# Optimization experiments

Measured on AMD Instinct MI355X. Metric: run time of the kernel, lower is better.

The kernel has to match this reference:

```python
import jax, jax.numpy as jnp
import numpy as np

B, S, H = 32, 2048, 512

def setup_inputs() -> dict:
    key = jax.random.key(0)
    k1, k2, k3, k4 = jax.random.split(key, 4)
    Y = jax.random.normal(k1, (B, S, H), dtype=jnp.float32)
    mask_Y = jnp.ones((B, S), dtype=jnp.float32)
    W = jax.random.normal(k2, (H, H), dtype=jnp.float32)
    b = jax.random.normal(k3, (H,), dtype=jnp.float32)
    w = jax.random.normal(k4, (H,), dtype=jnp.float32)
    return {"Y": Y, "mask_Y": mask_Y, "W": W, "b": b, "w": w}

def reference(Y, mask_Y, W, b, w):
    # u: [B,S,H] = tanh(Y @ W + b)
    u = jnp.tanh(jnp.einsum('bsh,hd->bsd', Y, W) + b)
    # scores: [B,S] = u . w, masked with large negative additive bias
    scores = jnp.einsum('bsh,h->bs', u, w) - 1000.0 * (1.0 - mask_Y)
    alpha = jax.nn.softmax(scores, axis=1)  # [B,S]
    # c_star: [B,H] = attention-weighted sum of Y
    c_star = jnp.einsum('bs,bsh->bh', alpha, Y)
    return c_star
```

## Files before the change

kernel.cpp:

```cpp
#include <hip/hip_runtime.h>
#include <hip/hip_bf16.h>


#define Bsz 32
#define Ssz 2048
#define Hsz 512
#define Msz (Bsz * Ssz)

using half8   = __attribute__((ext_vector_type(8))) _Float16;
using floatx4 = __attribute__((ext_vector_type(4))) float;

__device__ __forceinline__ void llds(_Float16* l, const _Float16* g) {
  __builtin_amdgcn_global_load_lds((const __attribute__((address_space(1))) void*)g,
                                   (__attribute__((address_space(3))) void*)l, 16, 0, 0);
}

__device__ __forceinline__ float fast_tanh(float x) {
  const float e = __expf(2.f * x);
  return 1.f - 2.f / (e + 1.f);
}

__global__ __launch_bounds__(256) void wsplit_k(const float* __restrict__ W,
                                                _Float16* __restrict__ Wt) {
  __shared__ float tile[32][33];
  const int bx = blockIdx.x & 15, by = blockIdx.x >> 4;
  const int tx = threadIdx.x & 31, ty = threadIdx.x >> 5;
#pragma unroll
  for (int i = 0; i < 4; ++i)
    tile[ty + 8 * i][tx] = W[(size_t)(by * 32 + ty + 8 * i) * Hsz + bx * 32 + tx];
  __syncthreads();
#pragma unroll
  for (int i = 0; i < 4; ++i) {
    const int n = bx * 32 + ty + 8 * i;
    const int k = by * 32 + tx;
    const float v = tile[tx][ty + 8 * i];
    const _Float16 hi = (_Float16)v;
    const _Float16 lo = (_Float16)(v - (float)hi);
    Wt[(size_t)n * 1024 + k] = hi;
    Wt[(size_t)n * 1024 + 512 + k] = lo;
  }
}

__global__ __launch_bounds__(256) void gemm_score_k(const float* __restrict__ Y,
                                                    const _Float16* __restrict__ Wt,
                                                    const float* __restrict__ bvec,
                                                    const float* __restrict__ wvec,
                                                    float* __restrict__ scores4) {
  __shared__ __align__(16) _Float16 As[128 * 32];
  __shared__ __align__(16) _Float16 Bh[128 * 32];
  __shared__ __align__(16) _Float16 Bl[128 * 32];
  const int tid = threadIdx.x;
  const int lane = tid & 63, wv = tid >> 6;
  const int wr = wv >> 1, wc = wv & 1;
  const int lr = lane & 15, lq = lane >> 4;
  const int g = blockIdx.x;
  const int x = g & 7, q = g >> 3;
  const int nblk = q & 3;
  const int mblk = (q >> 2) * 8 + x;

  floatx4 acc[4][4];
#pragma unroll
  for (int rf = 0; rf < 4; ++rf)
#pragma unroll
    for (int cf = 0; cf < 4; ++cf)
      acc[rf][cf] = (floatx4){0.f, 0.f, 0.f, 0.f};

  const int arow = tid >> 1;
  const int p0 = (tid & 1) * 2;
  const float* aga = Y + ((size_t)(mblk * 128 + arow)) * Hsz + p0 * 8;
  const int s0 = (p0 ^ ((arow >> 1) & 3)) * 8;
  const int s1 = ((p0 + 1) ^ ((arow >> 1) & 3)) * 8;
  const size_t brow0 = (size_t)nblk * 128 * 1024;

  for (int it = 0; it < 16; ++it) {
    const int k0 = it * 32;
#pragma unroll
    for (int i = 0; i < 2; ++i) {
      const int cbase = i * 256 + wv * 64;
      const int c = cbase + lane;
      const int brow = c >> 2;
      const int gpart = (c & 3) ^ ((c >> 3) & 3);
      const _Float16* gb = Wt + brow0 + (size_t)brow * 1024 + (k0 + gpart * 8);
      llds(&Bh[cbase * 8], gb);
      llds(&Bl[cbase * 8], gb + 512);
    }
    {
      const float4* g4 = (const float4*)(aga + k0);
      const float4 f0 = g4[0], f1 = g4[1], f2 = g4[2], f3 = g4[3];
      half8 h0, h1;
      h0[0] = (_Float16)f0.x; h0[1] = (_Float16)f0.y; h0[2] = (_Float16)f0.z; h0[3] = (_Float16)f0.w;
      h0[4] = (_Float16)f1.x; h0[5] = (_Float16)f1.y; h0[6] = (_Float16)f1.z; h0[7] = (_Float16)f1.w;
      h1[0] = (_Float16)f2.x; h1[1] = (_Float16)f2.y; h1[2] = (_Float16)f2.z; h1[3] = (_Float16)f2.w;
      h1[4] = (_Float16)f3.x; h1[5] = (_Float16)f3.y; h1[6] = (_Float16)f3.z; h1[7] = (_Float16)f3.w;
      *(half8*)&As[arow * 32 + s0] = h0;
      *(half8*)&As[arow * 32 + s1] = h1;
    }
    __syncthreads();

    half8 a[4], bhf[4], blf[4];
#pragma unroll
    for (int rf = 0; rf < 4; ++rf) {
      const int ar = wr * 64 + rf * 16 + lr;
      a[rf] = *(const half8*)&As[ar * 32 + (lq ^ ((ar >> 1) & 3)) * 8];
    }
#pragma unroll
    for (int cf = 0; cf < 4; ++cf) {
      const int nr = wc * 64 + cf * 16 + lr;
      const int na = nr * 32 + (lq ^ ((nr >> 1) & 3)) * 8;
      bhf[cf] = *(const half8*)&Bh[na];
      blf[cf] = *(const half8*)&Bl[na];
    }
#pragma unroll
    for (int rf = 0; rf < 4; ++rf)
#pragma unroll
      for (int cf = 0; cf < 4; ++cf)
        acc[rf][cf] = __builtin_amdgcn_mfma_f32_16x16x32_f16(a[rf], bhf[cf], acc[rf][cf], 0, 0, 0);
#pragma unroll
    for (int rf = 0; rf < 4; ++rf)
#pragma unroll
      for (int cf = 0; cf < 4; ++cf)
        acc[rf][cf] = __builtin_amdgcn_mfma_f32_16x16x32_f16(a[rf], blf[cf], acc[rf][cf], 0, 0, 0);
    __syncthreads();
  }

  float bb[4], ww[4];
  const int colbase = nblk * 128 + wc * 64;
#pragma unroll
  for (int cf = 0; cf < 4; ++cf) {
    const int col = colbase + cf * 16 + lr;
    bb[cf] = bvec[col];
    ww[cf] = wvec[col];
  }
  float* red = (float*)As;
#pragma unroll
  for (int rf = 0; rf < 4; ++rf) {
#pragma unroll
    for (int r = 0; r < 4; ++r) {
      float v = 0.f;
#pragma unroll
      for (int cf = 0; cf < 4; ++cf)
        v += fast_tanh(acc[rf][cf][r] + bb[cf]) * ww[cf];
      v += __shfl_xor(v, 1, 16);
      v += __shfl_xor(v, 2, 16);
      v += __shfl_xor(v, 4, 16);
      v += __shfl_xor(v, 8, 16);
      if (lr == 0)
        red[(wr * 64 + rf * 16 + lq * 4 + r) * 2 + wc] = v;
    }
  }
  __syncthreads();
  if (tid < 128)
    scores4[(size_t)nblk * Msz + mblk * 128 + tid] = red[2 * tid] + red[2 * tid + 1];
}

__global__ __launch_bounds__(256) void softmax_k(const float* __restrict__ scores4,
                                                 const float* __restrict__ mask,
                                                 float* __restrict__ alpha) {
  const int b = blockIdx.x, t = threadIdx.x;
  const int lane = t & 63, wv = t >> 6;
  float s[8];
  float mx = -3.4e38f;
#pragma unroll
  for (int i = 0; i < 8; ++i) {
    const int idx = b * Ssz + i * 256 + t;
    float v = scores4[idx] + scores4[Msz + idx] + scores4[2 * Msz + idx] + scores4[3 * Msz + idx];
    v -= 1000.f * (1.f - mask[idx]);
    s[i] = v;
    mx = fmaxf(mx, v);
  }
  for (int off = 32; off > 0; off >>= 1) mx = fmaxf(mx, __shfl_xor(mx, off, 64));
  __shared__ float rm[4], rs[4];
  if (lane == 0) rm[wv] = mx;
  __syncthreads();
  mx = fmaxf(fmaxf(rm[0], rm[1]), fmaxf(rm[2], rm[3]));
  float sum = 0.f;
#pragma unroll
  for (int i = 0; i < 8; ++i) {
    s[i] = __expf(s[i] - mx);
    sum += s[i];
  }
  for (int off = 32; off > 0; off >>= 1) sum += __shfl_xor(sum, off, 64);
  if (lane == 0) rs[wv] = sum;
  __syncthreads();
  sum = rs[0] + rs[1] + rs[2] + rs[3];
  const float inv = 1.f / sum;
#pragma unroll
  for (int i = 0; i < 8; ++i) alpha[b * Ssz + i * 256 + t] = s[i] * inv;
}

__global__ __launch_bounds__(256) void wsum_k(const float* __restrict__ alpha,
                                              const float* __restrict__ Y,
                                              float* __restrict__ out) {
  const int b = blockIdx.x >> 6, sc = blockIdx.x & 63;
  const int t = threadIdx.x;
  const float2* Y2 = (const float2*)(Y + ((size_t)b * Ssz + sc * 32) * Hsz);
  const float* al = alpha + b * Ssz + sc * 32;
  float cx = 0.f, cy = 0.f;
  for (int s = 0; s < 32; ++s) {
    const float a = al[s];
    const float2 y = Y2[(size_t)s * 256 + t];
    cx = fmaf(a, y.x, cx);
    cy = fmaf(a, y.y, cy);
  }
  atomicAdd(&out[b * Hsz + 2 * t], cx);
  atomicAdd(&out[b * Hsz + 2 * t + 1], cy);
}

extern "C" void kernel_launch(void* const* d_in, const int* in_sizes, int n_in,
                              void* d_out, int out_size, void* d_ws, size_t ws_size,
                              hipStream_t stream) {
  (void)in_sizes; (void)n_in; (void)out_size; (void)ws_size;
  const float* Y    = (const float*)d_in[0];
  const float* mask = (const float*)d_in[1];
  const float* W    = (const float*)d_in[2];
  const float* bvec = (const float*)d_in[3];
  const float* wvec = (const float*)d_in[4];
  float* out = (float*)d_out;

  char* ws = (char*)d_ws;
  _Float16* Wt   = (_Float16*)ws;
  float* scores4 = (float*)(ws + ((size_t)1 << 20));
  float* alpha   = (float*)(ws + ((size_t)2 << 20));

  hipMemsetAsync(out, 0, Bsz * Hsz * sizeof(float), stream);

  wsplit_k<<<256, 256, 0, stream>>>(W, Wt);
  gemm_score_k<<<(Msz / 128) * 4, 256, 0, stream>>>(Y, Wt, bvec, wvec, scores4);
  softmax_k<<<Bsz, 256, 0, stream>>>(scores4, mask, alpha);
  wsum_k<<<Bsz * 64, 256, 0, stream>>>(alpha, Y, out);
}
```

Before: 289.3 us.

## Double-buffer GEMM LDS tiles and fuse softmax into weighted-sum kernel

```diff
diff --git a/kernel.cpp b/kernel.cpp
--- a/kernel.cpp
+++ b/kernel.cpp
@@ -46,9 +46,9 @@
                                                     const float* __restrict__ bvec,
                                                     const float* __restrict__ wvec,
                                                     float* __restrict__ scores4) {
-  __shared__ __align__(16) _Float16 As[128 * 32];
-  __shared__ __align__(16) _Float16 Bh[128 * 32];
-  __shared__ __align__(16) _Float16 Bl[128 * 32];
+  __shared__ __align__(16) _Float16 As[2][128 * 32];
+  __shared__ __align__(16) _Float16 Bh[2][128 * 32];
+  __shared__ __align__(16) _Float16 Bl[2][128 * 32];
   const int tid = threadIdx.x;
   const int lane = tid & 63, wv = tid >> 6;
   const int wr = wv >> 1, wc = wv & 1;
@@ -72,7 +72,7 @@
   const int s1 = ((p0 + 1) ^ ((arow >> 1) & 3)) * 8;
   const size_t brow0 = (size_t)nblk * 128 * 1024;
 
-  for (int it = 0; it < 16; ++it) {
+  auto stageB = [&](int it, int buf) {
     const int k0 = it * 32;
 #pragma unroll
     for (int i = 0; i < 2; ++i) {
@@ -81,34 +81,52 @@
       const int brow = c >> 2;
       const int gpart = (c & 3) ^ ((c >> 3) & 3);
       const _Float16* gb = Wt + brow0 + (size_t)brow * 1024 + (k0 + gpart * 8);
-      llds(&Bh[cbase * 8], gb);
-      llds(&Bl[cbase * 8], gb + 512);
-    }
-    {
-      const float4* g4 = (const float4*)(aga + k0);
-      const float4 f0 = g4[0], f1 = g4[1], f2 = g4[2], f3 = g4[3];
-      half8 h0, h1;
-      h0[0] = (_Float16)f0.x; h0[1] = (_Float16)f0.y; h0[2] = (_Float16)f0.z; h0[3] = (_Float16)f0.w;
-      h0[4] = (_Float16)f1.x; h0[5] = (_Float16)f1.y; h0[6] = (_Float16)f1.z; h0[7] = (_Float16)f1.w;
-      h1[0] = (_Float16)f2.x; h1[1] = (_Float16)f2.y; h1[2] = (_Float16)f2.z; h1[3] = (_Float16)f2.w;
-      h1[4] = (_Float16)f3.x; h1[5] = (_Float16)f3.y; h1[6] = (_Float16)f3.z; h1[7] = (_Float16)f3.w;
-      *(half8*)&As[arow * 32 + s0] = h0;
-      *(half8*)&As[arow * 32 + s1] = h1;
-    }
+      llds(&Bh[buf][cbase * 8], gb);
+      llds(&Bl[buf][cbase * 8], gb + 512);
+    }
+  };
+  auto loadA = [&](int it, float4* f) {
+    const float4* g4 = (const float4*)(aga + it * 32);
+    f[0] = g4[0]; f[1] = g4[1]; f[2] = g4[2]; f[3] = g4[3];
+  };
+  auto cvtWriteA = [&](const float4* f, int buf) {
+    half8 h0, h1;
+    h0[0] = (_Float16)f[0].x; h0[1] = (_Float16)f[0].y; h0[2] = (_Float16)f[0].z; h0[3] = (_Float16)f[0].w;
+    h0[4] = (_Float16)f[1].x; h0[5] = (_Float16)f[1].y; h0[6] = (_Float16)f[1].z; h0[7] = (_Float16)f[1].w;
+    h1[0] = (_Float16)f[2].x; h1[1] = (_Float16)f[2].y; h1[2] = (_Float16)f[2].z; h1[3] = (_Float16)f[2].w;
+    h1[4] = (_Float16)f[3].x; h1[5] = (_Float16)f[3].y; h1[6] = (_Float16)f[3].z; h1[7] = (_Float16)f[3].w;
+    *(half8*)&As[buf][arow * 32 + s0] = h0;
+    *(half8*)&As[buf][arow * 32 + s1] = h1;
+  };
+
+  {
+    float4 fa[4];
+    stageB(0, 0);
+    loadA(0, fa);
+    cvtWriteA(fa, 0);
     __syncthreads();
+  }
+
+  for (int it = 0; it < 16; ++it) {
+    const int p = it & 1;
+    float4 fb[4];
+    if (it < 15) {
+      stageB(it + 1, p ^ 1);
+      loadA(it + 1, fb);
+    }
 
     half8 a[4], bhf[4], blf[4];
 #pragma unroll
     for (int rf = 0; rf < 4; ++rf) {
       const int ar = wr * 64 + rf * 16 + lr;
-      a[rf] = *(const half8*)&As[ar * 32 + (lq ^ ((ar >> 1) & 3)) * 8];
+      a[rf] = *(const half8*)&As[p][ar * 32 + (lq ^ ((ar >> 1) & 3)) * 8];
     }
 #pragma unroll
     for (int cf = 0; cf < 4; ++cf) {
       const int nr = wc * 64 + cf * 16 + lr;
       const int na = nr * 32 + (lq ^ ((nr >> 1) & 3)) * 8;
-      bhf[cf] = *(const half8*)&Bh[na];
-      blf[cf] = *(const half8*)&Bl[na];
+      bhf[cf] = *(const half8*)&Bh[p][na];
+      blf[cf] = *(const half8*)&Bl[p][na];
     }
 #pragma unroll
     for (int rf = 0; rf < 4; ++rf)
@@ -120,6 +138,9 @@
 #pragma unroll
       for (int cf = 0; cf < 4; ++cf)
         acc[rf][cf] = __builtin_amdgcn_mfma_f32_16x16x32_f16(a[rf], blf[cf], acc[rf][cf], 0, 0, 0);
+
+    if (it < 15)
+      cvtWriteA(fb, p ^ 1);
     __syncthreads();
   }
 
@@ -153,11 +174,16 @@
     scores4[(size_t)nblk * Msz + mblk * 128 + tid] = red[2 * tid] + red[2 * tid + 1];
 }
 
-__global__ __launch_bounds__(256) void softmax_k(const float* __restrict__ scores4,
-                                                 const float* __restrict__ mask,
-                                                 float* __restrict__ alpha) {
-  const int b = blockIdx.x, t = threadIdx.x;
-  const int lane = t & 63, wv = t >> 6;
+__global__ __launch_bounds__(256) void wsum_fused_k(const float* __restrict__ scores4,
+                                                    const float* __restrict__ mask,
+                                                    const float* __restrict__ Y,
+                                                    float* __restrict__ out) {
+  const int b = blockIdx.x >> 3, hs = blockIdx.x & 7;
+  const int t = threadIdx.x, lane = t & 63, wv = t >> 6;
+  __shared__ float alpha_s[Ssz];
+  __shared__ float rbuf[256];
+  __shared__ float rm[4], rs[4];
+
   float s[8];
   float mx = -3.4e38f;
 #pragma unroll
@@ -169,7 +195,6 @@
     mx = fmaxf(mx, v);
   }
   for (int off = 32; off > 0; off >>= 1) mx = fmaxf(mx, __shfl_xor(mx, off, 64));
-  __shared__ float rm[4], rs[4];
   if (lane == 0) rm[wv] = mx;
   __syncthreads();
   mx = fmaxf(fmaxf(rm[0], rm[1]), fmaxf(rm[2], rm[3]));
@@ -185,25 +210,20 @@
   sum = rs[0] + rs[1] + rs[2] + rs[3];
   const float inv = 1.f / sum;
 #pragma unroll
-  for (int i = 0; i < 8; ++i) alpha[b * Ssz + i * 256 + t] = s[i] * inv;
-}
-
-__global__ __launch_bounds__(256) void wsum_k(const float* __restrict__ alpha,
-                                              const float* __restrict__ Y,
-                                              float* __restrict__ out) {
-  const int b = blockIdx.x >> 6, sc = blockIdx.x & 63;
-  const int t = threadIdx.x;
-  const float2* Y2 = (const float2*)(Y + ((size_t)b * Ssz + sc * 32) * Hsz);
-  const float* al = alpha + b * Ssz + sc * 32;
-  float cx = 0.f, cy = 0.f;
-  for (int s = 0; s < 32; ++s) {
-    const float a = al[s];
-    const float2 y = Y2[(size_t)s * 256 + t];
-    cx = fmaf(a, y.x, cx);
-    cy = fmaf(a, y.y, cy);
-  }
-  atomicAdd(&out[b * Hsz + 2 * t], cx);
-  atomicAdd(&out[b * Hsz + 2 * t + 1], cy);
+  for (int i = 0; i < 8; ++i) alpha_s[i * 256 + t] = s[i] * inv;
+  __syncthreads();
+
+  const float* Yp = Y + (size_t)b * Ssz * Hsz + hs * 64 + lane;
+  const int sbase = wv * 512;
+  float acc = 0.f;
+#pragma unroll 8
+  for (int k = 0; k < 512; ++k)
+    acc = fmaf(alpha_s[sbase + k], Yp[(size_t)(sbase + k) * Hsz], acc);
+  rbuf[t] = acc;
+  __syncthreads();
+  if (wv == 0)
+    out[b * Hsz + hs * 64 + lane] =
+        rbuf[lane] + rbuf[64 + lane] + rbuf[128 + lane] + rbuf[192 + lane];
 }
 
 extern "C" void kernel_launch(void* const* d_in, const int* in_sizes, int n_in,
@@ -220,12 +240,8 @@
   char* ws = (char*)d_ws;
   _Float16* Wt   = (_Float16*)ws;
   float* scores4 = (float*)(ws + ((size_t)1 << 20));
-  float* alpha   = (float*)(ws + ((size_t)2 << 20));
-
-  hipMemsetAsync(out, 0, Bsz * Hsz * sizeof(float), stream);
 
   wsplit_k<<<256, 256, 0, stream>>>(W, Wt);
   gemm_score_k<<<(Msz / 128) * 4, 256, 0, stream>>>(Y, Wt, bvec, wvec, scores4);
-  softmax_k<<<Bsz, 256, 0, stream>>>(scores4, mask, alpha);
-  wsum_k<<<Bsz * 64, 256, 0, stream>>>(alpha, Y, out);
-}
+  wsum_fused_k<<<Bsz * 8, 256, 0, stream>>>(scores4, mask, Y, out);
+}
```

New measurement: 336.8 us. 16.4% more time.

## Drop fp16 hi/lo split of W and replace atomic weighted sum with two-stage reduction

Applied to the files above, without the earlier changes.

```diff
diff --git a/kernel.cpp b/kernel.cpp
--- a/kernel.cpp
+++ b/kernel.cpp
@@ -33,11 +33,7 @@
   for (int i = 0; i < 4; ++i) {
     const int n = bx * 32 + ty + 8 * i;
     const int k = by * 32 + tx;
-    const float v = tile[tx][ty + 8 * i];
-    const _Float16 hi = (_Float16)v;
-    const _Float16 lo = (_Float16)(v - (float)hi);
-    Wt[(size_t)n * 1024 + k] = hi;
-    Wt[(size_t)n * 1024 + 512 + k] = lo;
+    Wt[(size_t)n * Hsz + k] = (_Float16)tile[tx][ty + 8 * i];
   }
 }
 
@@ -48,7 +44,6 @@
                                                     float* __restrict__ scores4) {
   __shared__ __align__(16) _Float16 As[128 * 32];
   __shared__ __align__(16) _Float16 Bh[128 * 32];
-  __shared__ __align__(16) _Float16 Bl[128 * 32];
   const int tid = threadIdx.x;
   const int lane = tid & 63, wv = tid >> 6;
   const int wr = wv >> 1, wc = wv & 1;
@@ -70,19 +65,19 @@
   const float* aga = Y + ((size_t)(mblk * 128 + arow)) * Hsz + p0 * 8;
   const int s0 = (p0 ^ ((arow >> 1) & 3)) * 8;
   const int s1 = ((p0 + 1) ^ ((arow >> 1) & 3)) * 8;
-  const size_t brow0 = (size_t)nblk * 128 * 1024;
-
+  const size_t brow0 = (size_t)nblk * 128 * Hsz;
+
+  const int bc = wv * 64 + lane;
+  const int brow_a = bc >> 1;
   for (int it = 0; it < 16; ++it) {
     const int k0 = it * 32;
 #pragma unroll
     for (int i = 0; i < 2; ++i) {
-      const int cbase = i * 256 + wv * 64;
-      const int c = cbase + lane;
+      const int c = i * 256 + wv * 64 + lane;
       const int brow = c >> 2;
       const int gpart = (c & 3) ^ ((c >> 3) & 3);
-      const _Float16* gb = Wt + brow0 + (size_t)brow * 1024 + (k0 + gpart * 8);
-      llds(&Bh[cbase * 8], gb);
-      llds(&Bl[cbase * 8], gb + 512);
+      llds(&Bh[(i * 256 + wv * 64) * 8],
+           Wt + brow0 + (size_t)brow * Hsz + (k0 + gpart * 8));
     }
     {
       const float4* g4 = (const float4*)(aga + k0);
@@ -97,7 +92,7 @@
     }
     __syncthreads();
 
-    half8 a[4], bhf[4], blf[4];
+    half8 a[4], bhf[4];
 #pragma unroll
     for (int rf = 0; rf < 4; ++rf) {
       const int ar = wr * 64 + rf * 16 + lr;
@@ -106,20 +101,13 @@
 #pragma unroll
     for (int cf = 0; cf < 4; ++cf) {
       const int nr = wc * 64 + cf * 16 + lr;
-      const int na = nr * 32 + (lq ^ ((nr >> 1) & 3)) * 8;
-      bhf[cf] = *(const half8*)&Bh[na];
-      blf[cf] = *(const half8*)&Bl[na];
+      bhf[cf] = *(const half8*)&Bh[nr * 32 + (lq ^ ((nr >> 1) & 3)) * 8];
     }
 #pragma unroll
     for (int rf = 0; rf < 4; ++rf)
 #pragma unroll
       for (int cf = 0; cf < 4; ++cf)
         acc[rf][cf] = __builtin_amdgcn_mfma_f32_16x16x32_f16(a[rf], bhf[cf], acc[rf][cf], 0, 0, 0);
-#pragma unroll
-    for (int rf = 0; rf < 4; ++rf)
-#pragma unroll
-      for (int cf = 0; cf < 4; ++cf)
-        acc[rf][cf] = __builtin_amdgcn_mfma_f32_16x16x32_f16(a[rf], blf[cf], acc[rf][cf], 0, 0, 0);
     __syncthreads();
   }
 
@@ -188,22 +176,53 @@
   for (int i = 0; i < 8; ++i) alpha[b * Ssz + i * 256 + t] = s[i] * inv;
 }
 
-__global__ __launch_bounds__(256) void wsum_k(const float* __restrict__ alpha,
-                                              const float* __restrict__ Y,
-                                              float* __restrict__ out) {
-  const int b = blockIdx.x >> 6, sc = blockIdx.x & 63;
-  const int t = threadIdx.x;
-  const float2* Y2 = (const float2*)(Y + ((size_t)b * Ssz + sc * 32) * Hsz);
-  const float* al = alpha + b * Ssz + sc * 32;
-  float cx = 0.f, cy = 0.f;
-  for (int s = 0; s < 32; ++s) {
-    const float a = al[s];
-    const float2 y = Y2[(size_t)s * 256 + t];
-    cx = fmaf(a, y.x, cx);
-    cy = fmaf(a, y.y, cy);
-  }
-  atomicAdd(&out[b * Hsz + 2 * t], cx);
-  atomicAdd(&out[b * Hsz + 2 * t + 1], cy);
+__global__ __launch_bounds__(256) void wsum1_k(const float* __restrict__ alpha,
+                                               const float* __restrict__ Y,
+                                               float* __restrict__ partial) {
+  const int b = blockIdx.x >> 5, sc = blockIdx.x & 31;
+  const int t = threadIdx.x, lane = t & 63, wv = t >> 6;
+  __shared__ float part[4 * 512];
+  const int s0 = sc * 64 + wv * 16;
+  const float* al = alpha + b * Ssz + s0;
+  const float4* Yb = (const float4*)(Y + ((size_t)b * Ssz + s0) * Hsz);
+  float a0 = 0.f, a1 = 0.f, a2 = 0.f, a3 = 0.f, a4 = 0.f, a5 = 0.f, a6 = 0.f, a7 = 0.f;
+#pragma unroll 4
+  for (int r = 0; r < 16; ++r) {
+    const float a = al[r];
+    const float4 y0 = Yb[r * 128 + lane * 2];
+    const float4 y1 = Yb[r * 128 + lane * 2 + 1];
+    a0 = fmaf(a, y0.x, a0); a1 = fmaf(a, y0.y, a1);
+    a2 = fmaf(a, y0.z, a2); a3 = fmaf(a, y0.w, a3);
+    a4 = fmaf(a, y1.x, a4); a5 = fmaf(a, y1.y, a5);
+    a6 = fmaf(a, y1.z, a6); a7 = fmaf(a, y1.w, a7);
+  }
+  part[wv * 512 + 0 * 64 + lane] = a0;
+  part[wv * 512 + 1 * 64 + lane] = a1;
+  part[wv * 512 + 2 * 64 + lane] = a2;
+  part[wv * 512 + 3 * 64 + lane] = a3;
+  part[wv * 512 + 4 * 64 + lane] = a4;
+  part[wv * 512 + 5 * 64 + lane] = a5;
+  part[wv * 512 + 6 * 64 + lane] = a6;
+  part[wv * 512 + 7 * 64 + lane] = a7;
+  __syncthreads();
+#pragma unroll
+  for (int i = 0; i < 2; ++i) {
+    const int h = i * 256 + t;
+    const int idx = (h & 7) * 64 + (h >> 3);
+    partial[((size_t)(b * 32 + sc)) * Hsz + h] =
+        part[idx] + part[512 + idx] + part[1024 + idx] + part[1536 + idx];
+  }
+}
+
+__global__ __launch_bounds__(256) void wsum2_k(const float* __restrict__ partial,
+                                               float* __restrict__ out) {
+  const int b = blockIdx.x >> 1;
+  const int h = (blockIdx.x & 1) * 256 + threadIdx.x;
+  float s = 0.f;
+#pragma unroll 8
+  for (int sc = 0; sc < 32; ++sc)
+    s += partial[((size_t)(b * 32 + sc)) * Hsz + h];
+  out[b * Hsz + h] = s;
 }
 
 extern "C" void kernel_launch(void* const* d_in, const int* in_sizes, int n_in,
@@ -221,11 +240,11 @@
   _Float16* Wt   = (_Float16*)ws;
   float* scores4 = (float*)(ws + ((size_t)1 << 20));
   float* alpha   = (float*)(ws + ((size_t)2 << 20));
-
-  hipMemsetAsync(out, 0, Bsz * Hsz * sizeof(float), stream);
+  float* partial = (float*)(ws + ((size_t)2 << 20) + (512u << 10));
 
   wsplit_k<<<256, 256, 0, stream>>>(W, Wt);
   gemm_score_k<<<(Msz / 128) * 4, 256, 0, stream>>>(Y, Wt, bvec, wvec, scores4);
   softmax_k<<<Bsz, 256, 0, stream>>>(scores4, mask, alpha);
-  wsum_k<<<Bsz * 64, 256, 0, stream>>>(alpha, Y, out);
-}
+  wsum1_k<<<Bsz * 32, 256, 0, stream>>>(alpha, Y, partial);
+  wsum2_k<<<Bsz * 2, 256, 0, stream>>>(partial, out);
+}
```

Measured after the change: 274.4 us. -5.1%, faster.
